# Kernel optimization log

Measured on AMD Instinct MI355X. Metric: run time of the kernel, lower is better.

Reference implementation:

```python
import jax, jax.numpy as jnp
import numpy as np

N_ACT = 3  # [relu, tanh, sigmoid]


def setup_inputs() -> dict:
    key = jax.random.key(0)
    k1, k2, k3 = jax.random.split(key, 3)
    B, IN, OUT = 4096, 4096, 4096
    x = jax.random.normal(k1, (B, IN), dtype=jnp.float32)
    W = jax.random.normal(k2, (OUT, IN), dtype=jnp.float32)
    b = jax.random.normal(k3, (OUT,), dtype=jnp.float32)
    return {"x": x, "W": W, "b": b}


def reference(x, W, b):
    # Linear: y = x @ W^T + b  -> [B, OUT]
    y = jnp.einsum("bi,oi->bo", x, W) + b
    # Per-output-column criterion: mean over batch, then idx = int(mean % 3).
    # torch `%` on tensors is remainder with the divisor's sign (non-negative
    # here), and int() then truncates == floor for non-negative values.
    means = jnp.mean(y, axis=0)                        # [OUT]
    idx = jnp.mod(means, float(N_ACT)).astype(jnp.int32)  # [OUT] in {0,1,2}
    idx_b = idx[None, :]                               # broadcast over batch
    # Device-side branchless select among the three activations.
    out = jnp.where(
        idx_b == 0,
        jax.nn.relu(y),
        jnp.where(idx_b == 1, jnp.tanh(y), jax.nn.sigmoid(y)),
    )
    return out
```

## Files before the change

### kernel.cpp

```cpp
#include <hip/hip_runtime.h>
#include <hip/hip_bf16.h>
#include <math.h>

#define B_DIM   4096
#define IN_DIM  4096
#define OUT_DIM 4096

typedef __attribute__((ext_vector_type(8))) short  short8;
typedef __attribute__((ext_vector_type(4))) float  floatx4;

__device__ __forceinline__ ushort f2bf(float f) {
    unsigned b = __float_as_uint(f);
    return (ushort)((b + 0x7fffu + ((b >> 16) & 1u)) >> 16);
}

__global__ void cvt_x_colsum(const float* __restrict__ x, ushort* __restrict__ xb,
                             double* __restrict__ xbar_sum) {
    int c0 = blockIdx.x * 1024 + threadIdx.x * 4;
    int r0 = blockIdx.y * 16;
    double s0 = 0, s1 = 0, s2 = 0, s3 = 0;
#pragma unroll 4
    for (int r = 0; r < 16; ++r) {
        size_t off = (size_t)(r0 + r) * IN_DIM + c0;
        float4 v = *(const float4*)(x + off);
        ushort4 o;
        o.x = f2bf(v.x); o.y = f2bf(v.y); o.z = f2bf(v.z); o.w = f2bf(v.w);
        *(ushort4*)(xb + off) = o;
        s0 += (double)v.x; s1 += (double)v.y; s2 += (double)v.z; s3 += (double)v.w;
    }
    double* p = xbar_sum + c0;
    atomicAdd(p + 0, s0); atomicAdd(p + 1, s1);
    atomicAdd(p + 2, s2); atomicAdd(p + 3, s3);
}

__global__ void cvt_w_means(const float* __restrict__ W, const float* __restrict__ bias,
                            const double* __restrict__ xbar_sum, ushort* __restrict__ wb,
                            int* __restrict__ idx) {
    __shared__ double red4[4];
    int o = blockIdx.x;
    size_t base = (size_t)o * IN_DIM;
    double s = 0.0;
#pragma unroll
    for (int j = 0; j < 4; ++j) {
        int i = j * 1024 + threadIdx.x * 4;
        float4 v = *(const float4*)(W + base + i);
        ushort4 ob;
        ob.x = f2bf(v.x); ob.y = f2bf(v.y); ob.z = f2bf(v.z); ob.w = f2bf(v.w);
        *(ushort4*)(wb + base + i) = ob;
        double2 xv0 = *(const double2*)(xbar_sum + i);
        double2 xv1 = *(const double2*)(xbar_sum + i + 2);
        s += (double)v.x * xv0.x + (double)v.y * xv0.y
           + (double)v.z * xv1.x + (double)v.w * xv1.y;
    }
#pragma unroll
    for (int off = 32; off; off >>= 1) s += __shfl_down(s, off, 64);
    if ((threadIdx.x & 63) == 0) red4[threadIdx.x >> 6] = s;
    __syncthreads();
    if (threadIdx.x == 0) {
        double tot = red4[0] + red4[1] + red4[2] + red4[3];
        float mf = (float)(tot * (1.0 / (double)B_DIM) + (double)bias[o]);
        float md = fmodf(mf, 3.0f);
        if (md < 0.0f) md += 3.0f;
        idx[o] = (int)md;
    }
}

__global__ void __launch_bounds__(512, 2) gemm_bt_act(
    const ushort* __restrict__ A,
    const ushort* __restrict__ Bt,
    const float*  __restrict__ bias,
    const int*    __restrict__ idx,
    float*        __restrict__ out) {
    __shared__ __align__(16) ushort lds[4][2][256 * 32];

    const int t    = threadIdx.x;
    const int w    = t >> 6;
    const int l    = t & 63;
    const int quad = l >> 4;
    const int lrow = l & 15;
    const int wm   = w >> 2;
    const int wn   = w & 3;

    const int b   = blockIdx.x;
    const int xcd = b & 7;
    const int p   = b >> 3;
    const int m0  = ((xcd >> 1) * 4 + (p >> 3)) * 256;
    const int n0  = ((xcd & 1) * 8 + (p & 7)) * 256;

    const int K = IN_DIM;

    size_t aoff[2], boff[2];
    int    ldso[2];
#pragma unroll
    for (int j = 0; j < 2; ++j) {
        int chunk = j * 512 + t;
        int r     = chunk >> 2;
        int kb    = (chunk & 3) ^ ((r >> 1) & 3);
        aoff[j] = (size_t)(m0 + r) * K + kb * 8;
        boff[j] = (size_t)(n0 + r) * K + kb * 8;
        ldso[j] = chunk * 8;
    }

    const int kbsw  = (quad ^ ((lrow >> 1) & 3)) * 16;
    const int abase = (wm * 128 + lrow) * 64 + kbsw;
    const int bbase = (wn * 64 + lrow) * 64 + kbsw;

    floatx4 acc[8][4] = {};

#pragma unroll
    for (int pt = 0; pt < 3; ++pt) {
        int ks = pt * 32;
#pragma unroll
        for (int j = 0; j < 2; ++j) {
            __builtin_amdgcn_global_load_lds(
                (__attribute__((address_space(1))) void*)(A + aoff[j] + ks),
                (__attribute__((address_space(3))) void*)(&lds[pt][0][ldso[j]]), 16, 0, 0);
            __builtin_amdgcn_global_load_lds(
                (__attribute__((address_space(1))) void*)(Bt + boff[j] + ks),
                (__attribute__((address_space(3))) void*)(&lds[pt][1][ldso[j]]), 16, 0, 0);
        }
    }
    asm volatile("s_waitcnt vmcnt(8)" ::: "memory");
    __builtin_amdgcn_s_barrier();

#pragma unroll 1
    for (int kt = 0; kt < 128; ++kt) {
        const char* sa = (const char*)&lds[kt & 3][0][0];
        const char* sb = (const char*)&lds[kt & 3][1][0];
        const int nt   = (kt + 3) & 127;
        const int slot = (kt + 3) & 3;
        const int ks   = nt * 32;

        short8 af[8], bf[4];

#pragma unroll
        for (int mi = 0; mi < 4; ++mi)
            af[mi] = *(const short8*)(sa + abase + mi * 1024);
#pragma unroll
        for (int ni = 0; ni < 4; ++ni)
            bf[ni] = *(const short8*)(sb + bbase + ni * 1024);
#pragma unroll
        for (int j = 0; j < 2; ++j)
            __builtin_amdgcn_global_load_lds(
                (__attribute__((address_space(1))) void*)(A + aoff[j] + ks),
                (__attribute__((address_space(3))) void*)(&lds[slot][0][ldso[j]]), 16, 0, 0);

        __builtin_amdgcn_s_barrier();
        __builtin_amdgcn_s_setprio(1);
#pragma unroll
        for (int mi = 0; mi < 4; ++mi)
#pragma unroll
            for (int ni = 0; ni < 4; ++ni)
                acc[mi][ni] = __builtin_amdgcn_mfma_f32_16x16x32_bf16(
                    af[mi], bf[ni], acc[mi][ni], 0, 0, 0);
        __builtin_amdgcn_s_setprio(0);
        __builtin_amdgcn_s_barrier();

#pragma unroll
        for (int mi = 4; mi < 8; ++mi)
            af[mi] = *(const short8*)(sa + abase + mi * 1024);
#pragma unroll
        for (int j = 0; j < 2; ++j)
            __builtin_amdgcn_global_load_lds(
                (__attribute__((address_space(1))) void*)(Bt + boff[j] + ks),
                (__attribute__((address_space(3))) void*)(&lds[slot][1][ldso[j]]), 16, 0, 0);

        asm volatile("s_waitcnt vmcnt(8)" ::: "memory");
        __builtin_amdgcn_s_barrier();
        __builtin_amdgcn_s_setprio(1);
#pragma unroll
        for (int mi = 4; mi < 8; ++mi)
#pragma unroll
            for (int ni = 0; ni < 4; ++ni)
                acc[mi][ni] = __builtin_amdgcn_mfma_f32_16x16x32_bf16(
                    af[mi], bf[ni], acc[mi][ni], 0, 0, 0);
        __builtin_amdgcn_s_setprio(0);
        __builtin_amdgcn_s_barrier();
    }

#pragma unroll
    for (int ni = 0; ni < 4; ++ni) {
        int   col     = n0 + wn * 64 + ni * 16 + lrow;
        int   id      = idx[col];
        float bv      = bias[col];
        float a       = (id == 1) ? -2.0f : -1.0f;
        bool  isrelu  = (id == 0);
        bool  istanh  = (id == 1);
#pragma unroll
        for (int mi = 0; mi < 8; ++mi) {
            int rowb = m0 + wm * 128 + mi * 16 + quad * 4;
#pragma unroll
            for (int r = 0; r < 4; ++r) {
                float y   = acc[mi][ni][r] + bv;
                float e   = __expf(a * y);
                float s   = __builtin_amdgcn_rcpf(1.0f + e);
                float act = istanh ? fmaf(2.0f, s, -1.0f) : s;
                float v   = isrelu ? fmaxf(y, 0.0f) : act;
                out[(size_t)(rowb + r) * OUT_DIM + col] = v;
            }
        }
    }
}

extern "C" void kernel_launch(void* const* d_in, const int* in_sizes, int n_in,
                              void* d_out, int out_size, void* d_ws, size_t ws_size,
                              hipStream_t stream) {
    const float* x = (const float*)d_in[0];
    const float* W = (const float*)d_in[1];
    const float* b = (const float*)d_in[2];
    float* out = (float*)d_out;

    char* ws = (char*)d_ws;
    ushort* xb   = (ushort*)(ws);
    ushort* wb   = (ushort*)(ws + 33554432);
    double* xbar = (double*)(ws + 67108864);
    int*    idx  = (int*)   (ws + 67108864 + 32768);

    hipMemsetAsync(xbar, 0, IN_DIM * sizeof(double), stream);
    cvt_x_colsum<<<dim3(4, 256), 256, 0, stream>>>(x, xb, xbar);
    cvt_w_means<<<4096, 256, 0, stream>>>(W, b, xbar, wb, idx);
    gemm_bt_act<<<256, 512, 0, stream>>>(xb, wb, b, idx, out);
}
```

Before: 310.6 us.

## Switch GEMM to BK=64 double-buffered LDS pipeline with 8-way swizzle

Replaces the 4-stage BK=32 LDS ring with a 2-stage BK=64 double buffer, which halves the number of main-loop iterations and barrier rounds per unit of K. A/B tiles are staged in 128-row halves with an XOR swizzle over 8 groups of 16 bytes. The loop is split into four MFMA phases fenced by sched_barrier and explicit lgkmcnt/vmcnt waits. LDS use is unchanged at 128 KB, but prefetch depth drops to about one K-tile ahead and each iteration now has more barriers, which can expose global load latency.

```diff
diff --git a/kernel.cpp b/kernel.cpp
--- a/kernel.cpp
+++ b/kernel.cpp
@@ -71,7 +71,7 @@
     const float*  __restrict__ bias,
     const int*    __restrict__ idx,
     float*        __restrict__ out) {
-    __shared__ __align__(16) ushort lds[4][2][256 * 32];
+    __shared__ __align__(16) ushort lds[2][2][256 * 64];
 
     const int t    = threadIdx.x;
     const int w    = t >> 6;
@@ -89,101 +89,135 @@
 
     const int K = IN_DIM;
 
-    size_t aoff[2], boff[2];
-    int    ldso[2];
+    size_t aoffs[2], boffs[2];
+    int    ldsoff[2];
 #pragma unroll
     for (int j = 0; j < 2; ++j) {
-        int chunk = j * 512 + t;
-        int r     = chunk >> 2;
-        int kb    = (chunk & 3) ^ ((r >> 1) & 3);
-        aoff[j] = (size_t)(m0 + r) * K + kb * 8;
-        boff[j] = (size_t)(n0 + r) * K + kb * 8;
-        ldso[j] = chunk * 8;
-    }
-
-    const int kbsw  = (quad ^ ((lrow >> 1) & 3)) * 16;
-    const int abase = (wm * 128 + lrow) * 64 + kbsw;
-    const int bbase = (wn * 64 + lrow) * 64 + kbsw;
+        int c  = j * 512 + t;
+        int r  = c >> 3;
+        int lg = (c & 7) ^ (r & 7);
+        aoffs[j]  = (size_t)(m0 + r) * K + lg * 8;
+        boffs[j]  = (size_t)(n0 + r) * K + lg * 8;
+        ldsoff[j] = c * 8;
+    }
+
+#define STAGE(ptr, offs, mat, half, kt, slot)                                    \
+    {                                                                             \
+        _Pragma("unroll")                                                         \
+        for (int j = 0; j < 2; ++j)                                               \
+            __builtin_amdgcn_global_load_lds(                                     \
+                (__attribute__((address_space(1))) void*)((ptr) + offs[j] +       \
+                    (size_t)(half) * 128 * IN_DIM + (size_t)(kt) * 64),           \
+                (__attribute__((address_space(3))) void*)(&lds[slot][mat][(half) * 128 * 64 + ldsoff[j]]), \
+                16, 0, 0);                                                        \
+    }
+
+    const int gsw   = (quad ^ (lrow & 7)) << 4;
+    const int aBase = (wm * 128 + lrow) * 128 + gsw;
+    const int bBase = (wn * 64 + lrow) * 128 + gsw;
+    const int aBase1 = aBase ^ 64;
+    const int bBase1 = bBase ^ 64;
 
     floatx4 acc[8][4] = {};
 
-#pragma unroll
-    for (int pt = 0; pt < 3; ++pt) {
-        int ks = pt * 32;
-#pragma unroll
-        for (int j = 0; j < 2; ++j) {
-            __builtin_amdgcn_global_load_lds(
-                (__attribute__((address_space(1))) void*)(A + aoff[j] + ks),
-                (__attribute__((address_space(3))) void*)(&lds[pt][0][ldso[j]]), 16, 0, 0);
-            __builtin_amdgcn_global_load_lds(
-                (__attribute__((address_space(1))) void*)(Bt + boff[j] + ks),
-                (__attribute__((address_space(3))) void*)(&lds[pt][1][ldso[j]]), 16, 0, 0);
-        }
-    }
-    asm volatile("s_waitcnt vmcnt(8)" ::: "memory");
+    STAGE(Bt, boffs, 1, 0, 0, 0); STAGE(Bt, boffs, 1, 1, 0, 0);
+    STAGE(A,  aoffs, 0, 0, 0, 0); STAGE(A,  aoffs, 0, 1, 0, 0);
+    STAGE(Bt, boffs, 1, 0, 1, 1); STAGE(Bt, boffs, 1, 1, 1, 1);
+    asm volatile("s_waitcnt vmcnt(4)" ::: "memory");
     __builtin_amdgcn_s_barrier();
 
 #pragma unroll 1
-    for (int kt = 0; kt < 128; ++kt) {
-        const char* sa = (const char*)&lds[kt & 3][0][0];
-        const char* sb = (const char*)&lds[kt & 3][1][0];
-        const int nt   = (kt + 3) & 127;
-        const int slot = (kt + 3) & 3;
-        const int ks   = nt * 32;
-
-        short8 af[8], bf[4];
-
-#pragma unroll
-        for (int mi = 0; mi < 4; ++mi)
-            af[mi] = *(const short8*)(sa + abase + mi * 1024);
-#pragma unroll
-        for (int ni = 0; ni < 4; ++ni)
-            bf[ni] = *(const short8*)(sb + bbase + ni * 1024);
-#pragma unroll
-        for (int j = 0; j < 2; ++j)
-            __builtin_amdgcn_global_load_lds(
-                (__attribute__((address_space(1))) void*)(A + aoff[j] + ks),
-                (__attribute__((address_space(3))) void*)(&lds[slot][0][ldso[j]]), 16, 0, 0);
-
-        __builtin_amdgcn_s_barrier();
+    for (int k = 0; k < 64; ++k) {
+        const int s = k & 1, o = s ^ 1;
+        const char* sA = (const char*)&lds[s][0][0];
+        const char* sB = (const char*)&lds[s][1][0];
+        short8 a[4], bfr[4];
+
+#pragma unroll
+        for (int mi = 0; mi < 4; ++mi) a[mi]   = *(const short8*)(sA + aBase + mi * 2048);
+#pragma unroll
+        for (int ni = 0; ni < 4; ++ni) bfr[ni] = *(const short8*)(sB + bBase + ni * 2048);
+        if (k + 1 < 64) STAGE(A, aoffs, 0, 0, k + 1, o);
+        __builtin_amdgcn_sched_barrier(0);
+        __builtin_amdgcn_s_barrier();
+        asm volatile("s_waitcnt lgkmcnt(0)" ::: "memory");
+        __builtin_amdgcn_sched_barrier(0);
         __builtin_amdgcn_s_setprio(1);
 #pragma unroll
         for (int mi = 0; mi < 4; ++mi)
 #pragma unroll
             for (int ni = 0; ni < 4; ++ni)
                 acc[mi][ni] = __builtin_amdgcn_mfma_f32_16x16x32_bf16(
-                    af[mi], bf[ni], acc[mi][ni], 0, 0, 0);
-        __builtin_amdgcn_s_setprio(0);
-        __builtin_amdgcn_s_barrier();
-
-#pragma unroll
-        for (int mi = 4; mi < 8; ++mi)
-            af[mi] = *(const short8*)(sa + abase + mi * 1024);
-#pragma unroll
-        for (int j = 0; j < 2; ++j)
-            __builtin_amdgcn_global_load_lds(
-                (__attribute__((address_space(1))) void*)(Bt + boff[j] + ks),
-                (__attribute__((address_space(3))) void*)(&lds[slot][1][ldso[j]]), 16, 0, 0);
-
-        asm volatile("s_waitcnt vmcnt(8)" ::: "memory");
-        __builtin_amdgcn_s_barrier();
-        __builtin_amdgcn_s_setprio(1);
-#pragma unroll
-        for (int mi = 4; mi < 8; ++mi)
+                    a[mi], bfr[ni], acc[mi][ni], 0, 0, 0);
+        __builtin_amdgcn_s_setprio(0);
+        __builtin_amdgcn_sched_barrier(0);
+        __builtin_amdgcn_s_barrier();
+
+#pragma unroll
+        for (int mi = 0; mi < 4; ++mi) a[mi] = *(const short8*)(sA + aBase + (mi + 4) * 2048);
+        if (k + 1 < 64) STAGE(A, aoffs, 0, 1, k + 1, o);
+        __builtin_amdgcn_sched_barrier(0);
+        __builtin_amdgcn_s_barrier();
+        asm volatile("s_waitcnt lgkmcnt(0)" ::: "memory");
+        __builtin_amdgcn_sched_barrier(0);
+        __builtin_amdgcn_s_setprio(1);
+#pragma unroll
+        for (int mi = 0; mi < 4; ++mi)
+#pragma unroll
+            for (int ni = 0; ni < 4; ++ni)
+                acc[mi + 4][ni] = __builtin_amdgcn_mfma_f32_16x16x32_bf16(
+                    a[mi], bfr[ni], acc[mi + 4][ni], 0, 0, 0);
+        __builtin_amdgcn_s_setprio(0);
+        __builtin_amdgcn_sched_barrier(0);
+        __builtin_amdgcn_s_barrier();
+
+#pragma unroll
+        for (int mi = 0; mi < 4; ++mi) a[mi]   = *(const short8*)(sA + aBase1 + mi * 2048);
+#pragma unroll
+        for (int ni = 0; ni < 4; ++ni) bfr[ni] = *(const short8*)(sB + bBase1 + ni * 2048);
+        __builtin_amdgcn_sched_barrier(0);
+        __builtin_amdgcn_s_barrier();
+        asm volatile("s_waitcnt lgkmcnt(0)" ::: "memory");
+        __builtin_amdgcn_sched_barrier(0);
+        __builtin_amdgcn_s_setprio(1);
+#pragma unroll
+        for (int mi = 0; mi < 4; ++mi)
 #pragma unroll
             for (int ni = 0; ni < 4; ++ni)
                 acc[mi][ni] = __builtin_amdgcn_mfma_f32_16x16x32_bf16(
-                    af[mi], bf[ni], acc[mi][ni], 0, 0, 0);
-        __builtin_amdgcn_s_setprio(0);
-        __builtin_amdgcn_s_barrier();
-    }
+                    a[mi], bfr[ni], acc[mi][ni], 0, 0, 0);
+        __builtin_amdgcn_s_setprio(0);
+        __builtin_amdgcn_sched_barrier(0);
+        __builtin_amdgcn_s_barrier();
+
+#pragma unroll
+        for (int mi = 0; mi < 4; ++mi) a[mi] = *(const short8*)(sA + aBase1 + (mi + 4) * 2048);
+        if (k + 2 < 64) { STAGE(Bt, boffs, 1, 0, k + 2, s); STAGE(Bt, boffs, 1, 1, k + 2, s); }
+        if (k < 62) { asm volatile("s_waitcnt vmcnt(4)" ::: "memory"); }
+        else        { asm volatile("s_waitcnt vmcnt(0)" ::: "memory"); }
+        __builtin_amdgcn_sched_barrier(0);
+        __builtin_amdgcn_s_barrier();
+        asm volatile("s_waitcnt lgkmcnt(0)" ::: "memory");
+        __builtin_amdgcn_sched_barrier(0);
+        __builtin_amdgcn_s_setprio(1);
+#pragma unroll
+        for (int mi = 0; mi < 4; ++mi)
+#pragma unroll
+            for (int ni = 0; ni < 4; ++ni)
+                acc[mi + 4][ni] = __builtin_amdgcn_mfma_f32_16x16x32_bf16(
+                    a[mi], bfr[ni], acc[mi + 4][ni], 0, 0, 0);
+        __builtin_amdgcn_s_setprio(0);
+        __builtin_amdgcn_sched_barrier(0);
+        __builtin_amdgcn_s_barrier();
+    }
+#undef STAGE
 
 #pragma unroll
     for (int ni = 0; ni < 4; ++ni) {
         int   col     = n0 + wn * 64 + ni * 16 + lrow;
         int   id      = idx[col];
         float bv      = bias[col];
-        float a       = (id == 1) ? -2.0f : -1.0f;
+        float aa      = (id == 1) ? -2.0f : -1.0f;
         bool  isrelu  = (id == 0);
         bool  istanh  = (id == 1);
 #pragma unroll
@@ -192,9 +226,9 @@
 #pragma unroll
             for (int r = 0; r < 4; ++r) {
                 float y   = acc[mi][ni][r] + bv;
-                float e   = __expf(a * y);
-                float s   = __builtin_amdgcn_rcpf(1.0f + e);
-                float act = istanh ? fmaf(2.0f, s, -1.0f) : s;
+                float e   = __expf(aa * y);
+                float sg  = __builtin_amdgcn_rcpf(1.0f + e);
+                float act = istanh ? fmaf(2.0f, sg, -1.0f) : sg;
                 float v   = isrelu ? fmaxf(y, 0.0f) : act;
                 out[(size_t)(rowb + r) * OUT_DIM + col] = v;
             }
```

New measurement: 310.2 us. Within noise of the previous version (-0.1%).

## Shrink GEMM tile to 128x256 with 4 waves and 3-stage single-barrier pipeline

Applied to the files above, without the earlier changes.

The GEMM moves from 256x256 tiles with 8 waves and a 4-slot LDS ring to 128x256 tiles with 4 waves per block, 512 blocks, and a 3-slot ring. Each K step now has one wait and one barrier, and all MFMAs of a step run together instead of in two halves. The change is meant to cut per-step synchronisation and raise the number of resident blocks. In exchange, each block reuses less data, so A/B traffic per FLOP goes up. Separately, the x-conversion kernel now processes 64 rows per block, which reduces the number of double atomics.

```diff
diff --git a/kernel.cpp b/kernel.cpp
--- a/kernel.cpp
+++ b/kernel.cpp
@@ -17,10 +17,10 @@
 __global__ void cvt_x_colsum(const float* __restrict__ x, ushort* __restrict__ xb,
                              double* __restrict__ xbar_sum) {
     int c0 = blockIdx.x * 1024 + threadIdx.x * 4;
-    int r0 = blockIdx.y * 16;
+    int r0 = blockIdx.y * 64;
     double s0 = 0, s1 = 0, s2 = 0, s3 = 0;
-#pragma unroll 4
-    for (int r = 0; r < 16; ++r) {
+#pragma unroll 8
+    for (int r = 0; r < 64; ++r) {
         size_t off = (size_t)(r0 + r) * IN_DIM + c0;
         float4 v = *(const float4*)(x + off);
         ushort4 o;
@@ -65,136 +65,118 @@
     }
 }
 
-__global__ void __launch_bounds__(512, 2) gemm_bt_act(
+__global__ void __launch_bounds__(256, 2) gemm_bt_act(
     const ushort* __restrict__ A,
     const ushort* __restrict__ Bt,
     const float*  __restrict__ bias,
     const int*    __restrict__ idx,
     float*        __restrict__ out) {
-    __shared__ __align__(16) ushort lds[4][2][256 * 32];
+    __shared__ __align__(16) ushort lds[3][12288];
 
     const int t    = threadIdx.x;
     const int w    = t >> 6;
     const int l    = t & 63;
     const int quad = l >> 4;
     const int lrow = l & 15;
-    const int wm   = w >> 2;
-    const int wn   = w & 3;
 
     const int b   = blockIdx.x;
     const int xcd = b & 7;
     const int p   = b >> 3;
-    const int m0  = ((xcd >> 1) * 4 + (p >> 3)) * 256;
+    const int m0  = ((xcd >> 1) * 8 + (p >> 3)) * 128;
     const int n0  = ((xcd & 1) * 8 + (p & 7)) * 256;
 
     const int K = IN_DIM;
 
-    size_t aoff[2], boff[2];
-    int    ldso[2];
+    size_t aoff[2];  int alds[2];
+    size_t boff[4];  int blds[4];
 #pragma unroll
     for (int j = 0; j < 2; ++j) {
-        int chunk = j * 512 + t;
-        int r     = chunk >> 2;
-        int kb    = (chunk & 3) ^ ((r >> 1) & 3);
-        aoff[j] = (size_t)(m0 + r) * K + kb * 8;
-        boff[j] = (size_t)(n0 + r) * K + kb * 8;
-        ldso[j] = chunk * 8;
+        int c  = j * 256 + t;
+        int r  = c >> 2;
+        int pg = (c & 3) ^ ((r >> 1) & 3);
+        aoff[j] = (size_t)(m0 + r) * K + pg * 8;
+        alds[j] = c * 8;
+    }
+#pragma unroll
+    for (int j = 0; j < 4; ++j) {
+        int c  = j * 256 + t;
+        int r  = c >> 2;
+        int pg = (c & 3) ^ ((r >> 1) & 3);
+        boff[j] = (size_t)(n0 + r) * K + pg * 8;
+        blds[j] = 4096 + c * 8;
     }
 
     const int kbsw  = (quad ^ ((lrow >> 1) & 3)) * 16;
-    const int abase = (wm * 128 + lrow) * 64 + kbsw;
-    const int bbase = (wn * 64 + lrow) * 64 + kbsw;
+    const int aBase = lrow * 64 + kbsw;
+    const int bBase = 8192 + (w * 64 + lrow) * 64 + kbsw;
 
     floatx4 acc[8][4] = {};
 
-#pragma unroll
-    for (int pt = 0; pt < 3; ++pt) {
-        int ks = pt * 32;
-#pragma unroll
-        for (int j = 0; j < 2; ++j) {
-            __builtin_amdgcn_global_load_lds(
-                (__attribute__((address_space(1))) void*)(A + aoff[j] + ks),
-                (__attribute__((address_space(3))) void*)(&lds[pt][0][ldso[j]]), 16, 0, 0);
-            __builtin_amdgcn_global_load_lds(
-                (__attribute__((address_space(1))) void*)(Bt + boff[j] + ks),
-                (__attribute__((address_space(3))) void*)(&lds[pt][1][ldso[j]]), 16, 0, 0);
-        }
-    }
-    asm volatile("s_waitcnt vmcnt(8)" ::: "memory");
-    __builtin_amdgcn_s_barrier();
+#define STAGE(kt, slot)                                                          \
+    {                                                                             \
+        const size_t ks = (size_t)(kt) * 32;                                      \
+        _Pragma("unroll")                                                         \
+        for (int j = 0; j < 2; ++j)                                               \
+            __builtin_amdgcn_global_load_lds(                                     \
+                (__attribute__((address_space(1))) void*)(A + aoff[j] + ks),      \
+                (__attribute__((address_space(3))) void*)(&lds[slot][alds[j]]),   \
+                16, 0, 0);                                                        \
+        _Pragma("unroll")                                                         \
+        for (int j = 0; j < 4; ++j)                                               \
+            __builtin_amdgcn_global_load_lds(                                     \
+                (__attribute__((address_space(1))) void*)(Bt + boff[j] + ks),     \
+                (__attribute__((address_space(3))) void*)(&lds[slot][blds[j]]),   \
+                16, 0, 0);                                                        \
+    }
+
+    STAGE(0, 0);
+    STAGE(1, 1);
 
 #pragma unroll 1
     for (int kt = 0; kt < 128; ++kt) {
-        const char* sa = (const char*)&lds[kt & 3][0][0];
-        const char* sb = (const char*)&lds[kt & 3][1][0];
-        const int nt   = (kt + 3) & 127;
-        const int slot = (kt + 3) & 3;
-        const int ks   = nt * 32;
-
+        if (kt < 127) { asm volatile("s_waitcnt vmcnt(6)" ::: "memory"); }
+        else          { asm volatile("s_waitcnt vmcnt(0)" ::: "memory"); }
+        __builtin_amdgcn_s_barrier();
+
+        if (kt + 2 < 128) STAGE(kt + 2, (kt + 2) % 3);
+
+        const char* s = (const char*)&lds[kt % 3][0];
         short8 af[8], bf[4];
-
-#pragma unroll
-        for (int mi = 0; mi < 4; ++mi)
-            af[mi] = *(const short8*)(sa + abase + mi * 1024);
+#pragma unroll
+        for (int mi = 0; mi < 8; ++mi)
+            af[mi] = *(const short8*)(s + aBase + mi * 1024);
 #pragma unroll
         for (int ni = 0; ni < 4; ++ni)
-            bf[ni] = *(const short8*)(sb + bbase + ni * 1024);
-#pragma unroll
-        for (int j = 0; j < 2; ++j)
-            __builtin_amdgcn_global_load_lds(
-                (__attribute__((address_space(1))) void*)(A + aoff[j] + ks),
-                (__attribute__((address_space(3))) void*)(&lds[slot][0][ldso[j]]), 16, 0, 0);
-
-        __builtin_amdgcn_s_barrier();
+            bf[ni] = *(const short8*)(s + bBase + ni * 1024);
+
         __builtin_amdgcn_s_setprio(1);
 #pragma unroll
-        for (int mi = 0; mi < 4; ++mi)
+        for (int mi = 0; mi < 8; ++mi)
 #pragma unroll
             for (int ni = 0; ni < 4; ++ni)
                 acc[mi][ni] = __builtin_amdgcn_mfma_f32_16x16x32_bf16(
                     af[mi], bf[ni], acc[mi][ni], 0, 0, 0);
         __builtin_amdgcn_s_setprio(0);
-        __builtin_amdgcn_s_barrier();
-
-#pragma unroll
-        for (int mi = 4; mi < 8; ++mi)
-            af[mi] = *(const short8*)(sa + abase + mi * 1024);
-#pragma unroll
-        for (int j = 0; j < 2; ++j)
-            __builtin_amdgcn_global_load_lds(
-                (__attribute__((address_space(1))) void*)(Bt + boff[j] + ks),
-                (__attribute__((address_space(3))) void*)(&lds[slot][1][ldso[j]]), 16, 0, 0);
-
-        asm volatile("s_waitcnt vmcnt(8)" ::: "memory");
-        __builtin_amdgcn_s_barrier();
-        __builtin_amdgcn_s_setprio(1);
-#pragma unroll
-        for (int mi = 4; mi < 8; ++mi)
-#pragma unroll
-            for (int ni = 0; ni < 4; ++ni)
-                acc[mi][ni] = __builtin_amdgcn_mfma_f32_16x16x32_bf16(
-                    af[mi], bf[ni], acc[mi][ni], 0, 0, 0);
-        __builtin_amdgcn_s_setprio(0);
-        __builtin_amdgcn_s_barrier();
-    }
+    }
+#undef STAGE
 
 #pragma unroll
     for (int ni = 0; ni < 4; ++ni) {
-        int   col     = n0 + wn * 64 + ni * 16 + lrow;
+        int   col     = n0 + w * 64 + ni * 16 + lrow;
         int   id      = idx[col];
         float bv      = bias[col];
-        float a       = (id == 1) ? -2.0f : -1.0f;
+        float aa      = (id == 1) ? -2.0f : -1.0f;
         bool  isrelu  = (id == 0);
         bool  istanh  = (id == 1);
 #pragma unroll
         for (int mi = 0; mi < 8; ++mi) {
-            int rowb = m0 + wm * 128 + mi * 16 + quad * 4;
+            int rowb = m0 + mi * 16 + quad * 4;
 #pragma unroll
             for (int r = 0; r < 4; ++r) {
                 float y   = acc[mi][ni][r] + bv;
-                float e   = __expf(a * y);
-                float s   = __builtin_amdgcn_rcpf(1.0f + e);
-                float act = istanh ? fmaf(2.0f, s, -1.0f) : s;
+                float e   = __expf(aa * y);
+                float sg  = __builtin_amdgcn_rcpf(1.0f + e);
+                float act = istanh ? fmaf(2.0f, sg, -1.0f) : sg;
                 float v   = isrelu ? fmaxf(y, 0.0f) : act;
                 out[(size_t)(rowb + r) * OUT_DIM + col] = v;
             }
@@ -217,7 +199,7 @@
     int*    idx  = (int*)   (ws + 67108864 + 32768);
 
     hipMemsetAsync(xbar, 0, IN_DIM * sizeof(double), stream);
-    cvt_x_colsum<<<dim3(4, 256), 256, 0, stream>>>(x, xb, xbar);
+    cvt_x_colsum<<<dim3(4, 64), 256, 0, stream>>>(x, xb, xbar);
     cvt_w_means<<<4096, 256, 0, stream>>>(W, b, xbar, wb, idx);
-    gemm_bt_act<<<256, 512, 0, stream>>>(xb, wb, b, idx, out);
-}
+    gemm_bt_act<<<512, 256, 0, stream>>>(xb, wb, b, idx, out);
+}
```

Result: slower. 328.5 us (+5.7%).

## Merge bf16 conversions, split mean computation, simplify GEMM loop to one barrier

Applied to the files above, without the earlier changes.

The x and W float-to-bf16 conversions now run in a single launch. A separate kernel computes the column means and activation indices, caching the x column sums in LDS and re-reading W in fp32. The GEMM main loop now uses one wait and barrier per K-step: it issues the next stage's A and B loads together, then loads all fragments and runs all 32 MFMAs, instead of splitting the step into two halves with interleaved loads. This cuts barrier count and launch serialization, but the means kernel reads W a second time, and the loop loses the finer interleaving of LDS reads, global loads and MFMAs.

```diff
diff --git a/kernel.cpp b/kernel.cpp
--- a/kernel.cpp
+++ b/kernel.cpp
@@ -14,54 +14,68 @@
     return (ushort)((b + 0x7fffu + ((b >> 16) & 1u)) >> 16);
 }
 
-__global__ void cvt_x_colsum(const float* __restrict__ x, ushort* __restrict__ xb,
-                             double* __restrict__ xbar_sum) {
-    int c0 = blockIdx.x * 1024 + threadIdx.x * 4;
-    int r0 = blockIdx.y * 16;
+__global__ void cvt_both(const float* __restrict__ x, const float* __restrict__ W,
+                         ushort* __restrict__ xb, ushort* __restrict__ wb,
+                         double* __restrict__ xbar_sum) {
+    const int  bid = blockIdx.x;
+    const bool isx = bid < 1024;
+    const int  lb  = isx ? bid : bid - 1024;
+    const int  c0  = (lb & 3) * 1024 + threadIdx.x * 4;
+    const int  r0  = (lb >> 2) * 16;
+    const float* src = isx ? x  : W;
+    ushort*      dst = isx ? xb : wb;
     double s0 = 0, s1 = 0, s2 = 0, s3 = 0;
 #pragma unroll 4
     for (int r = 0; r < 16; ++r) {
         size_t off = (size_t)(r0 + r) * IN_DIM + c0;
-        float4 v = *(const float4*)(x + off);
+        float4 v = *(const float4*)(src + off);
         ushort4 o;
         o.x = f2bf(v.x); o.y = f2bf(v.y); o.z = f2bf(v.z); o.w = f2bf(v.w);
-        *(ushort4*)(xb + off) = o;
-        s0 += (double)v.x; s1 += (double)v.y; s2 += (double)v.z; s3 += (double)v.w;
-    }
-    double* p = xbar_sum + c0;
-    atomicAdd(p + 0, s0); atomicAdd(p + 1, s1);
-    atomicAdd(p + 2, s2); atomicAdd(p + 3, s3);
-}
-
-__global__ void cvt_w_means(const float* __restrict__ W, const float* __restrict__ bias,
-                            const double* __restrict__ xbar_sum, ushort* __restrict__ wb,
-                            int* __restrict__ idx) {
+        *(ushort4*)(dst + off) = o;
+        if (isx) {
+            s0 += (double)v.x; s1 += (double)v.y;
+            s2 += (double)v.z; s3 += (double)v.w;
+        }
+    }
+    if (isx) {
+        double* p = xbar_sum + c0;
+        atomicAdd(p + 0, s0); atomicAdd(p + 1, s1);
+        atomicAdd(p + 2, s2); atomicAdd(p + 3, s3);
+    }
+}
+
+__global__ void means_idx(const float* __restrict__ W, const float* __restrict__ bias,
+                          const double* __restrict__ xbar_sum, int* __restrict__ idx) {
+    __shared__ double xs[4096];
     __shared__ double red4[4];
-    int o = blockIdx.x;
-    size_t base = (size_t)o * IN_DIM;
-    double s = 0.0;
-#pragma unroll
-    for (int j = 0; j < 4; ++j) {
-        int i = j * 1024 + threadIdx.x * 4;
-        float4 v = *(const float4*)(W + base + i);
-        ushort4 ob;
-        ob.x = f2bf(v.x); ob.y = f2bf(v.y); ob.z = f2bf(v.z); ob.w = f2bf(v.w);
-        *(ushort4*)(wb + base + i) = ob;
-        double2 xv0 = *(const double2*)(xbar_sum + i);
-        double2 xv1 = *(const double2*)(xbar_sum + i + 2);
-        s += (double)v.x * xv0.x + (double)v.y * xv0.y
-           + (double)v.z * xv1.x + (double)v.w * xv1.y;
-    }
-#pragma unroll
-    for (int off = 32; off; off >>= 1) s += __shfl_down(s, off, 64);
-    if ((threadIdx.x & 63) == 0) red4[threadIdx.x >> 6] = s;
+#pragma unroll
+    for (int j = 0; j < 16; ++j)
+        xs[j * 256 + threadIdx.x] = xbar_sum[j * 256 + threadIdx.x];
     __syncthreads();
-    if (threadIdx.x == 0) {
-        double tot = red4[0] + red4[1] + red4[2] + red4[3];
-        float mf = (float)(tot * (1.0 / (double)B_DIM) + (double)bias[o]);
-        float md = fmodf(mf, 3.0f);
-        if (md < 0.0f) md += 3.0f;
-        idx[o] = (int)md;
+    const int o0 = blockIdx.x * 8;
+    for (int rr = 0; rr < 8; ++rr) {
+        const int o = o0 + rr;
+        size_t base = (size_t)o * IN_DIM;
+        double s = 0.0;
+#pragma unroll
+        for (int j = 0; j < 4; ++j) {
+            int i = j * 1024 + threadIdx.x * 4;
+            float4 v = *(const float4*)(W + base + i);
+            s += (double)v.x * xs[i]     + (double)v.y * xs[i + 1]
+               + (double)v.z * xs[i + 2] + (double)v.w * xs[i + 3];
+        }
+#pragma unroll
+        for (int off = 32; off; off >>= 1) s += __shfl_down(s, off, 64);
+        if ((threadIdx.x & 63) == 0) red4[threadIdx.x >> 6] = s;
+        __syncthreads();
+        if (threadIdx.x == 0) {
+            double tot = red4[0] + red4[1] + red4[2] + red4[3];
+            float mf = (float)(tot * (1.0 / (double)B_DIM) + (double)bias[o]);
+            float md = fmodf(mf, 3.0f);
+            if (md < 0.0f) md += 3.0f;
+            idx[o] = (int)md;
+        }
+        __syncthreads();
     }
 }
 
@@ -120,62 +134,45 @@
                 (__attribute__((address_space(3))) void*)(&lds[pt][1][ldso[j]]), 16, 0, 0);
         }
     }
-    asm volatile("s_waitcnt vmcnt(8)" ::: "memory");
-    __builtin_amdgcn_s_barrier();
 
 #pragma unroll 1
     for (int kt = 0; kt < 128; ++kt) {
+        asm volatile("s_waitcnt vmcnt(8)" ::: "memory");
+        __builtin_amdgcn_s_barrier();
+
+        {
+            int nt   = (kt + 3) & 127;
+            int slot = (kt + 3) & 3;
+            int ks   = nt * 32;
+#pragma unroll
+            for (int j = 0; j < 2; ++j) {
+                __builtin_amdgcn_global_load_lds(
+                    (__attribute__((address_space(1))) void*)(A + aoff[j] + ks),
+                    (__attribute__((address_space(3))) void*)(&lds[slot][0][ldso[j]]), 16, 0, 0);
+                __builtin_amdgcn_global_load_lds(
+                    (__attribute__((address_space(1))) void*)(Bt + boff[j] + ks),
+                    (__attribute__((address_space(3))) void*)(&lds[slot][1][ldso[j]]), 16, 0, 0);
+            }
+        }
+
         const char* sa = (const char*)&lds[kt & 3][0][0];
         const char* sb = (const char*)&lds[kt & 3][1][0];
-        const int nt   = (kt + 3) & 127;
-        const int slot = (kt + 3) & 3;
-        const int ks   = nt * 32;
-
         short8 af[8], bf[4];
-
-#pragma unroll
-        for (int mi = 0; mi < 4; ++mi)
+#pragma unroll
+        for (int mi = 0; mi < 8; ++mi)
             af[mi] = *(const short8*)(sa + abase + mi * 1024);
 #pragma unroll
         for (int ni = 0; ni < 4; ++ni)
             bf[ni] = *(const short8*)(sb + bbase + ni * 1024);
-#pragma unroll
-        for (int j = 0; j < 2; ++j)
-            __builtin_amdgcn_global_load_lds(
-                (__attribute__((address_space(1))) void*)(A + aoff[j] + ks),
-                (__attribute__((address_space(3))) void*)(&lds[slot][0][ldso[j]]), 16, 0, 0);
-
-        __builtin_amdgcn_s_barrier();
+
         __builtin_amdgcn_s_setprio(1);
 #pragma unroll
-        for (int mi = 0; mi < 4; ++mi)
+        for (int mi = 0; mi < 8; ++mi)
 #pragma unroll
             for (int ni = 0; ni < 4; ++ni)
                 acc[mi][ni] = __builtin_amdgcn_mfma_f32_16x16x32_bf16(
                     af[mi], bf[ni], acc[mi][ni], 0, 0, 0);
         __builtin_amdgcn_s_setprio(0);
-        __builtin_amdgcn_s_barrier();
-
-#pragma unroll
-        for (int mi = 4; mi < 8; ++mi)
-            af[mi] = *(const short8*)(sa + abase + mi * 1024);
-#pragma unroll
-        for (int j = 0; j < 2; ++j)
-            __builtin_amdgcn_global_load_lds(
-                (__attribute__((address_space(1))) void*)(Bt + boff[j] + ks),
-                (__attribute__((address_space(3))) void*)(&lds[slot][1][ldso[j]]), 16, 0, 0);
-
-        asm volatile("s_waitcnt vmcnt(8)" ::: "memory");
-        __builtin_amdgcn_s_barrier();
-        __builtin_amdgcn_s_setprio(1);
-#pragma unroll
-        for (int mi = 4; mi < 8; ++mi)
-#pragma unroll
-            for (int ni = 0; ni < 4; ++ni)
-                acc[mi][ni] = __builtin_amdgcn_mfma_f32_16x16x32_bf16(
-                    af[mi], bf[ni], acc[mi][ni], 0, 0, 0);
-        __builtin_amdgcn_s_setprio(0);
-        __builtin_amdgcn_s_barrier();
     }
 
 #pragma unroll
@@ -217,7 +214,7 @@
     int*    idx  = (int*)   (ws + 67108864 + 32768);
 
     hipMemsetAsync(xbar, 0, IN_DIM * sizeof(double), stream);
-    cvt_x_colsum<<<dim3(4, 256), 256, 0, stream>>>(x, xb, xbar);
-    cvt_w_means<<<4096, 256, 0, stream>>>(W, b, xbar, wb, idx);
+    cvt_both<<<2048, 256, 0, stream>>>(x, W, xb, wb, xbar);
+    means_idx<<<512, 256, 0, stream>>>(W, b, xbar, idx);
     gemm_bt_act<<<256, 512, 0, stream>>>(xb, wb, b, idx, out);
 }
```

After: 334.1 us. 1.08x slower.
